# Performance work log

Hardware: AMD Instinct MI355X
Metric: run time of the kernel (lower is better)

## Reference

```python
import jax, jax.numpy as jnp
import numpy as np

K = 2            # negative:positive edge ratio (init arg k)
N_NODES = 4096
N_EDGES = 8192
FEAT = 64


def setup_inputs() -> dict:
    key = jax.random.key(0)
    k1, k2, k3 = jax.random.split(key, 3)
    node_feature = jax.random.normal(k1, (N_NODES, FEAT), dtype=jnp.float32)
    edge_src = jax.random.randint(k2, (N_EDGES,), 0, N_NODES, dtype=jnp.int32)
    edge_dst = jax.random.randint(k3, (N_EDGES,), 0, N_NODES, dtype=jnp.int32)
    return {"node_feature": node_feature, "edge_src": edge_src, "edge_dst": edge_dst}


def reference(node_feature, edge_src, edge_dst):
    E = edge_src.shape[0]
    N = node_feature.shape[0]
    # [E, E] pairwise mask: candidate column j is valid for row i iff
    # dst[j] != dst[i] and dst[j] != src[i]
    valid = (edge_dst[:, None] != edge_dst[None, :]) & (edge_src[:, None] != edge_dst[None, :])
    # unsorted_segment_min over rows grouped by edge_src -> [N, E]
    segmin = jax.ops.segment_min(valid.astype(jnp.int8), edge_src, num_segments=N)
    # gather back per edge -> [E, E], flatten
    m = segmin[edge_src].reshape(-1).astype(bool)  # [E*E]
    num_negatives = jnp.sum(m)
    ratio = num_negatives // E                      # integer ratio as in TF code
    keep_prob = (K / ratio).astype(jnp.float32)
    u = jax.random.uniform(jax.random.key(42), (E * E,), dtype=jnp.float32)
    keep = m & (u < keep_prob)
    # fixed-size (jit-friendly) stand-in for tf.boolean_mask: expected count is K*E;
    # pad/truncate to exactly K*E kept flat indices (fill_value=0 pads).
    idx = jnp.nonzero(keep, size=K * E, fill_value=0)[0]
    rows = idx // E
    cols = idx % E
    edge_src_neg = edge_src[rows]
    edge_dst_neg = edge_dst[cols]
    return edge_src_neg, edge_dst_neg
```

## Files before the change

### kernel.cpp

```cpp
#include <hip/hip_runtime.h>
#include <stdint.h>
#include <math.h>

typedef unsigned int u32;
typedef unsigned long long u64;

#define E_CNT   8192
#define N_CNT   4096
#define TOT_N   (1u << 26)
#define OUT_K   16384
#define NODE_BM_WORDS 128
#define N_CHUNKS 1024

#define OFF_BAD      0x000000
#define OFF_CNT_DST  0x200000
#define OFF_CNT_SRC  0x204000
#define OFF_CCOUNT   0x208000
#define OFF_SCALARS  0x209000
#define OFF_KEEPBM   0x210000
#define ZERO_BYTES   0x209040

__device__ __forceinline__ u32 rotl32(u32 x, u32 d) {
  return __builtin_amdgcn_alignbit(x, x, 32u - d);
}

__device__ __forceinline__ void threefry2_0_42(u32 ia, u32 ib, u32& bits_a, u32& bits_b) {
  const u32 k1 = 42u, k2 = 0x1BD11BF0u;
  u32 a0 = ia + k1, a1r;
  u32 b0 = ib + k1;
  u32 A0 = 0u, A1 = a0;
  u32 B0 = 0u, B1 = b0;
#define R2(r) { A0 += A1; B0 += B1; A1 = rotl32(A1, r); B1 = rotl32(B1, r); A1 ^= A0; B1 ^= B0; }
  R2(13) R2(15) R2(26) R2(6)
  A0 += k1; B0 += k1; A1 += k2 + 1u; B1 += k2 + 1u;
  R2(17) R2(29) R2(16) R2(24)
  A0 += k2; B0 += k2; A1 += 2u; B1 += 2u;
  R2(13) R2(15) R2(26) R2(6)
   A1 += k1 + 3u; B1 += k1 + 3u;
  R2(17) R2(29) R2(16) R2(24)
  A0 += k1; B0 += k1; A1 += k2 + 4u; B1 += k2 + 4u;
  R2(13) R2(15) R2(26) R2(6)
  A0 += k2; B0 += k2; A1 += 5u; B1 += 5u;
#undef R2
  bits_a = A0 ^ A1;
  bits_b = B0 ^ B1;
  (void)a1r;
}

__global__ void k_build(const int* __restrict__ src, const int* __restrict__ dst,
                        u32* __restrict__ bad, u32* __restrict__ cnt_dst,
                        u32* __restrict__ cnt_src, int* __restrict__ out) {
  int tid = blockIdx.x * 256 + threadIdx.x;
  if (tid < N_CNT) {
    atomicOr(&bad[(u32)tid * NODE_BM_WORDS + ((u32)tid >> 5)], 1u << (tid & 31));
  }
  u32 s = (u32)src[tid], d = (u32)dst[tid];
  atomicOr(&bad[s * NODE_BM_WORDS + (d >> 5)], 1u << (d & 31));
  atomicAdd(&cnt_dst[d], 1u);
  atomicAdd(&cnt_src[s], 1u);
  int s0 = src[0], d0 = dst[0];
  out[tid] = s0;            out[tid + E_CNT] = s0;
  out[OUT_K + tid] = d0;    out[OUT_K + tid + E_CNT] = d0;
}

__global__ void __launch_bounds__(1024) k_rowcount(const u32* __restrict__ bad,
                                                   const u32* __restrict__ cnt_dst,
                                                   const u32* __restrict__ cnt_src,
                                                   u32* __restrict__ scal) {
  int wv = threadIdx.x >> 6, ln = threadIdx.x & 63;
  int n = blockIdx.x * 16 + wv;
  const u32* row = bad + (u32)n * NODE_BM_WORDS;
  u32 sum = 0;
#pragma unroll
  for (int h = 0; h < 2; ++h) {
    int w = ln + h * 64;
    u32 bits = row[w];
    while (bits) { int b = __ffs(bits) - 1; sum += cnt_dst[(w << 5) + b]; bits &= bits - 1; }
  }
#pragma unroll
  for (int off = 32; off > 0; off >>= 1) sum += __shfl_down(sum, off, 64);
  __shared__ u32 part[16];
  if (ln == 0) part[wv] = ((u32)E_CNT - sum) * cnt_src[n];
  __syncthreads();
  if (threadIdx.x == 0) {
    u32 tot = 0;
#pragma unroll
    for (int k = 0; k < 16; ++k) tot += part[k];
    atomicAdd(&scal[0], tot);
    __threadfence();
    if (atomicAdd(&scal[1], 1u) == 255u) {
      u32 nn = atomicAdd(&scal[0], 0u);
      u32 ratio = nn >> 13;
      float kp = 2.0f / (float)ratio;
      u32 T = (u32)ceil((double)kp * 8388608.0);
      u32 T9 = (T >= (1u << 23)) ? 0xFFFFFFFFu : (T << 9);
      atomicExch(&scal[2], T9);
    }
  }
}

__global__ void __launch_bounds__(256) k_sample(const int* __restrict__ src,
                                                const int* __restrict__ dst,
                                                const u32* __restrict__ bad,
                                                const u32* __restrict__ scal,
                                                u64* __restrict__ keep_bm,
                                                u32* __restrict__ ccount) {
  u32 wv = threadIdx.x >> 6, ln = threadIdx.x & 63;
  u32 i0w = blockIdx.x * 2048u + wv * 512u;
  u32 T9 = scal[2];
  u64 words[8];
  u64 any = 0;
#pragma unroll
  for (int j = 0; j < 4; ++j) {
    u32 ia = i0w + (u32)j * 128u + ln;
    u32 ba, bb;
    threefry2_0_42(ia, ia + 64u, ba, bb);
    u64 ma = __ballot(ba < T9);
    u64 mb = __ballot(bb < T9);
    words[2 * j] = ma; words[2 * j + 1] = mb;
    any |= ma | mb;
  }
  if (any) {
#pragma unroll
    for (int k = 0; k < 8; ++k) {
      if (words[k]) {
        u32 i = i0w + (u32)k * 64u + ln;
        bool kp = (words[k] >> ln) & 1ull;
        if (kp) {
          u32 n = (u32)src[i >> 13]; u32 v = (u32)dst[i & 8191];
          kp = ((bad[n * NODE_BM_WORDS + (v >> 5)] >> (v & 31)) & 1u) == 0u;
        }
        words[k] = __ballot(kp);
      }
    }
  }
  if (ln == 0) {
    u32 widx = i0w >> 6;
    ulonglong2* p = (ulonglong2*)&keep_bm[widx];
    p[0] = make_ulonglong2(words[0], words[1]);
    p[1] = make_ulonglong2(words[2], words[3]);
    p[2] = make_ulonglong2(words[4], words[5]);
    p[3] = make_ulonglong2(words[6], words[7]);
    u32 c = 0;
#pragma unroll
    for (int k = 0; k < 8; ++k) c += (u32)__popcll(words[k]);
    if (c) atomicAdd(&ccount[i0w >> 16], c);
  }
}

__global__ void k_compact(const int* __restrict__ src, const int* __restrict__ dst,
                          const u64* __restrict__ keep_bm, const u32* __restrict__ ccount,
                          int* __restrict__ out) {
  int c = blockIdx.x;
  int t = threadIdx.x;
  __shared__ u32 s[256];
  __shared__ u32 base_sh;

  u32 v[4]; u32 sum4 = 0;
#pragma unroll
  for (int k = 0; k < 4; ++k) { v[k] = ccount[4 * t + k]; sum4 += v[k]; }
  s[t] = sum4; __syncthreads();
  for (int off = 1; off < 256; off <<= 1) {
    u32 x = (t >= off) ? s[t - off] : 0u;
    __syncthreads();
    s[t] += x;
    __syncthreads();
  }
  if (t == (c >> 2)) {
    u32 excl = s[t] - sum4;
#pragma unroll
    for (int k = 0; k < 4; ++k) if (k < (c & 3)) excl += v[k];
    base_sh = excl;
  }
  __syncthreads();
  u32 coff_c = base_sh;
  __syncthreads();

  const u64* words = keep_bm + (size_t)c * 1024;
  u64 w[4];
  u32 cnt = 0;
#pragma unroll
  for (int k = 0; k < 4; ++k) { w[k] = words[4 * t + k]; cnt += (u32)__popcll(w[k]); }
  s[t] = cnt; __syncthreads();
  for (int off = 1; off < 256; off <<= 1) {
    u32 x = (t >= off) ? s[t - off] : 0u;
    __syncthreads();
    s[t] += x;
    __syncthreads();
  }
  u32 rank = coff_c + s[t] - cnt;
  u32 tbase = (u32)c * 65536u + (u32)t * 256u;
#pragma unroll
  for (int k = 0; k < 4; ++k) {
    u64 bits = w[k];
    while (bits) {
      int b = __ffsll((unsigned long long)bits) - 1;
      if (rank < OUT_K) {
        u32 tt = tbase + (u32)k * 64u + (u32)b;
        out[rank]         = src[tt >> 13];
        out[OUT_K + rank] = dst[tt & 8191];
      }
      rank++;
      bits &= bits - 1;
    }
  }
}

extern "C" void kernel_launch(void* const* d_in, const int* in_sizes, int n_in,
                              void* d_out, int out_size, void* d_ws, size_t ws_size,
                              hipStream_t stream) {
  const int* src = (const int*)d_in[1];
  const int* dst = (const int*)d_in[2];
  int* out = (int*)d_out;
  char* ws = (char*)d_ws;

  u32* bad     = (u32*)(ws + OFF_BAD);
  u32* cnt_dst = (u32*)(ws + OFF_CNT_DST);
  u32* cnt_src = (u32*)(ws + OFF_CNT_SRC);
  u32* ccount  = (u32*)(ws + OFF_CCOUNT);
  u32* scal    = (u32*)(ws + OFF_SCALARS);
  u64* keep_bm = (u64*)(ws + OFF_KEEPBM);

  hipMemsetAsync(ws, 0, ZERO_BYTES, stream);
  k_build<<<E_CNT / 256, 256, 0, stream>>>(src, dst, bad, cnt_dst, cnt_src, out);
  k_rowcount<<<N_CNT / 16, 1024, 0, stream>>>(bad, cnt_dst, cnt_src, scal);
  k_sample<<<TOT_N / 2048, 256, 0, stream>>>(src, dst, bad, scal, keep_bm, ccount);
  k_compact<<<N_CHUNKS, 256, 0, stream>>>(src, dst, keep_bm, ccount, out);
}
```

Baseline: 189.1 us.

## Fuse build, rowcount, sample and compact into one persistent kernel with grid barriers

```diff
diff --git a/kernel.cpp b/kernel.cpp
--- a/kernel.cpp
+++ b/kernel.cpp
@@ -7,10 +7,11 @@
 
 #define E_CNT   8192
 #define N_CNT   4096
-#define TOT_N   (1u << 26)
 #define OUT_K   16384
 #define NODE_BM_WORDS 128
-#define N_CHUNKS 1024
+#define NB      512
+#define NT      1024
+#define ELEMS_PER_BLOCK 131072u
 
 #define OFF_BAD      0x000000
 #define OFF_CNT_DST  0x200000
@@ -18,7 +19,7 @@
 #define OFF_CCOUNT   0x208000
 #define OFF_SCALARS  0x209000
 #define OFF_KEEPBM   0x210000
-#define ZERO_BYTES   0x209040
+#define ZERO_WORDS   (0x208000 / 4)
 
 __device__ __forceinline__ u32 rotl32(u32 x, u32 d) {
   return __builtin_amdgcn_alignbit(x, x, 32u - d);
@@ -26,17 +27,15 @@
 
 __device__ __forceinline__ void threefry2_0_42(u32 ia, u32 ib, u32& bits_a, u32& bits_b) {
   const u32 k1 = 42u, k2 = 0x1BD11BF0u;
-  u32 a0 = ia + k1, a1r;
-  u32 b0 = ib + k1;
-  u32 A0 = 0u, A1 = a0;
-  u32 B0 = 0u, B1 = b0;
+  u32 A0 = 0u, A1 = ia + k1;
+  u32 B0 = 0u, B1 = ib + k1;
 #define R2(r) { A0 += A1; B0 += B1; A1 = rotl32(A1, r); B1 = rotl32(B1, r); A1 ^= A0; B1 ^= B0; }
   R2(13) R2(15) R2(26) R2(6)
   A0 += k1; B0 += k1; A1 += k2 + 1u; B1 += k2 + 1u;
   R2(17) R2(29) R2(16) R2(24)
   A0 += k2; B0 += k2; A1 += 2u; B1 += 2u;
   R2(13) R2(15) R2(26) R2(6)
-   A1 += k1 + 3u; B1 += k1 + 3u;
+  A1 += k1 + 3u; B1 += k1 + 3u;
   R2(17) R2(29) R2(16) R2(24)
   A0 += k1; B0 += k1; A1 += k2 + 4u; B1 += k2 + 4u;
   R2(13) R2(15) R2(26) R2(6)
@@ -44,51 +43,95 @@
 #undef R2
   bits_a = A0 ^ A1;
   bits_b = B0 ^ B1;
-  (void)a1r;
-}
-
-__global__ void k_build(const int* __restrict__ src, const int* __restrict__ dst,
-                        u32* __restrict__ bad, u32* __restrict__ cnt_dst,
-                        u32* __restrict__ cnt_src, int* __restrict__ out) {
-  int tid = blockIdx.x * 256 + threadIdx.x;
-  if (tid < N_CNT) {
-    atomicOr(&bad[(u32)tid * NODE_BM_WORDS + ((u32)tid >> 5)], 1u << (tid & 31));
-  }
-  u32 s = (u32)src[tid], d = (u32)dst[tid];
-  atomicOr(&bad[s * NODE_BM_WORDS + (d >> 5)], 1u << (d & 31));
-  atomicAdd(&cnt_dst[d], 1u);
-  atomicAdd(&cnt_src[s], 1u);
-  int s0 = src[0], d0 = dst[0];
-  out[tid] = s0;            out[tid + E_CNT] = s0;
-  out[OUT_K + tid] = d0;    out[OUT_K + tid + E_CNT] = d0;
-}
-
-__global__ void __launch_bounds__(1024) k_rowcount(const u32* __restrict__ bad,
-                                                   const u32* __restrict__ cnt_dst,
-                                                   const u32* __restrict__ cnt_src,
-                                                   u32* __restrict__ scal) {
-  int wv = threadIdx.x >> 6, ln = threadIdx.x & 63;
-  int n = blockIdx.x * 16 + wv;
-  const u32* row = bad + (u32)n * NODE_BM_WORDS;
-  u32 sum = 0;
-#pragma unroll
-  for (int h = 0; h < 2; ++h) {
-    int w = ln + h * 64;
-    u32 bits = row[w];
-    while (bits) { int b = __ffs(bits) - 1; sum += cnt_dst[(w << 5) + b]; bits &= bits - 1; }
-  }
-#pragma unroll
-  for (int off = 32; off > 0; off >>= 1) sum += __shfl_down(sum, off, 64);
+}
+
+__device__ __forceinline__ void gbar(u32* bar) {
+  __syncthreads();
+  if (threadIdx.x == 0) {
+    __threadfence();
+    atomicAdd(bar, 1u);
+    while (atomicAdd(bar, 0u) < (u32)NB) __builtin_amdgcn_s_sleep(2);
+    __threadfence();
+  }
+  __syncthreads();
+}
+
+__device__ __forceinline__ u32 block_scan(u32 v, u32* s) {
+  int t = threadIdx.x;
+  s[t] = v; __syncthreads();
+  for (int off = 1; off < NT; off <<= 1) {
+    u32 x = (t >= off) ? s[t - off] : 0u;
+    __syncthreads();
+    s[t] += x;
+    __syncthreads();
+  }
+  u32 r = s[t];
+  __syncthreads();
+  return r;
+}
+
+__global__ void __launch_bounds__(NT, 8) k_all(const int* __restrict__ src,
+                                               const int* __restrict__ dst,
+                                               u32* __restrict__ ws32,
+                                               u64* __restrict__ keep_bm,
+                                               int* __restrict__ out) {
+  u32* bad     = ws32 + (OFF_BAD >> 2);
+  u32* cnt_dst = ws32 + (OFF_CNT_DST >> 2);
+  u32* cnt_src = ws32 + (OFF_CNT_SRC >> 2);
+  u32* ccount  = ws32 + (OFF_CCOUNT >> 2);
+  u32* scal    = ws32 + (OFF_SCALARS >> 2);
+  u32* bars    = scal + 3;
+
+  const u32 b = blockIdx.x, t = threadIdx.x;
+  const u32 wv = t >> 6, ln = t & 63;
+  const u32 g = b * NT + t;
+
+  __shared__ u32 s[NT];
   __shared__ u32 part[16];
-  if (ln == 0) part[wv] = ((u32)E_CNT - sum) * cnt_src[n];
-  __syncthreads();
-  if (threadIdx.x == 0) {
+  __shared__ u32 wsum[16];
+  __shared__ u32 sh_t9;
+  __shared__ u32 chunk_off[2];
+
+  ws32[g] = 0;
+  if (g < (u32)(ZERO_WORDS - NB * NT)) ws32[NB * NT + g] = 0;
+  gbar(&bars[0]);
+
+  if (g < N_CNT) atomicOr(&bad[g * NODE_BM_WORDS + (g >> 5)], 1u << (g & 31));
+  if (g < E_CNT) {
+    u32 sv = (u32)src[g], dv = (u32)dst[g];
+    atomicOr(&bad[sv * NODE_BM_WORDS + (dv >> 5)], 1u << (dv & 31));
+    atomicAdd(&cnt_dst[dv], 1u);
+    atomicAdd(&cnt_src[sv], 1u);
+    int s0 = src[0], d0 = dst[0];
+    out[g] = s0;           out[g + E_CNT] = s0;
+    out[OUT_K + g] = d0;   out[OUT_K + g + E_CNT] = d0;
+  }
+  gbar(&bars[1]);
+
+  if (t < 16) part[t] = 0;
+  __syncthreads();
+  u32 gw = b * 16 + wv;
+  if (gw < N_CNT) {
+    const u32* row = bad + gw * NODE_BM_WORDS;
+    u32 sum = 0;
+#pragma unroll
+    for (int h = 0; h < 2; ++h) {
+      u32 w = ln + h * 64u;
+      u32 bits = row[w];
+      while (bits) { int bb = __ffs(bits) - 1; sum += cnt_dst[(w << 5) + bb]; bits &= bits - 1; }
+    }
+#pragma unroll
+    for (int off = 32; off > 0; off >>= 1) sum += __shfl_down(sum, off, 64);
+    if (ln == 0) part[wv] = ((u32)E_CNT - sum) * cnt_src[gw];
+  }
+  __syncthreads();
+  if (t == 0) {
     u32 tot = 0;
 #pragma unroll
     for (int k = 0; k < 16; ++k) tot += part[k];
-    atomicAdd(&scal[0], tot);
+    if (tot) atomicAdd(&scal[0], tot);
     __threadfence();
-    if (atomicAdd(&scal[1], 1u) == 255u) {
+    if (atomicAdd(&scal[1], 1u) == (u32)(NB - 1)) {
       u32 nn = atomicAdd(&scal[0], 0u);
       u32 ratio = nn >> 13;
       float kp = 2.0f / (float)ratio;
@@ -97,111 +140,85 @@
       atomicExch(&scal[2], T9);
     }
   }
-}
-
-__global__ void __launch_bounds__(256) k_sample(const int* __restrict__ src,
-                                                const int* __restrict__ dst,
-                                                const u32* __restrict__ bad,
-                                                const u32* __restrict__ scal,
-                                                u64* __restrict__ keep_bm,
-                                                u32* __restrict__ ccount) {
-  u32 wv = threadIdx.x >> 6, ln = threadIdx.x & 63;
-  u32 i0w = blockIdx.x * 2048u + wv * 512u;
-  u32 T9 = scal[2];
-  u64 words[8];
-  u64 any = 0;
-#pragma unroll
-  for (int j = 0; j < 4; ++j) {
-    u32 ia = i0w + (u32)j * 128u + ln;
-    u32 ba, bb;
-    threefry2_0_42(ia, ia + 64u, ba, bb);
-    u64 ma = __ballot(ba < T9);
-    u64 mb = __ballot(bb < T9);
-    words[2 * j] = ma; words[2 * j + 1] = mb;
-    any |= ma | mb;
-  }
-  if (any) {
-#pragma unroll
-    for (int k = 0; k < 8; ++k) {
-      if (words[k]) {
-        u32 i = i0w + (u32)k * 64u + ln;
-        bool kp = (words[k] >> ln) & 1ull;
-        if (kp) {
-          u32 n = (u32)src[i >> 13]; u32 v = (u32)dst[i & 8191];
-          kp = ((bad[n * NODE_BM_WORDS + (v >> 5)] >> (v & 31)) & 1u) == 0u;
+  gbar(&bars[2]);
+  if (t == 0) sh_t9 = atomicAdd(&scal[2], 0u);
+  __syncthreads();
+  const u32 T9 = sh_t9;
+
+  const u32 eb = b * ELEMS_PER_BLOCK + wv * 8192u;
+  u32 wave_c = 0;
+  for (int it = 0; it < 16; ++it) {
+    u32 i0w = eb + (u32)it * 512u;
+    u64 words[8];
+    u64 any = 0;
+#pragma unroll
+    for (int j = 0; j < 4; ++j) {
+      u32 ia = i0w + (u32)j * 128u + ln;
+      u32 ba, bb;
+      threefry2_0_42(ia, ia + 64u, ba, bb);
+      u64 ma = __ballot(ba < T9);
+      u64 mb = __ballot(bb < T9);
+      words[2 * j] = ma; words[2 * j + 1] = mb;
+      any |= ma | mb;
+    }
+    if (any) {
+#pragma unroll
+      for (int k = 0; k < 8; ++k) {
+        if (words[k]) {
+          u32 i = i0w + (u32)k * 64u + ln;
+          bool kp = (words[k] >> ln) & 1ull;
+          if (kp) {
+            u32 n = (u32)src[i >> 13]; u32 v = (u32)dst[i & 8191];
+            kp = ((bad[n * NODE_BM_WORDS + (v >> 5)] >> (v & 31)) & 1u) == 0u;
+          }
+          words[k] = __ballot(kp);
         }
-        words[k] = __ballot(kp);
       }
     }
-  }
-  if (ln == 0) {
-    u32 widx = i0w >> 6;
-    ulonglong2* p = (ulonglong2*)&keep_bm[widx];
-    p[0] = make_ulonglong2(words[0], words[1]);
-    p[1] = make_ulonglong2(words[2], words[3]);
-    p[2] = make_ulonglong2(words[4], words[5]);
-    p[3] = make_ulonglong2(words[6], words[7]);
-    u32 c = 0;
-#pragma unroll
-    for (int k = 0; k < 8; ++k) c += (u32)__popcll(words[k]);
-    if (c) atomicAdd(&ccount[i0w >> 16], c);
-  }
-}
-
-__global__ void k_compact(const int* __restrict__ src, const int* __restrict__ dst,
-                          const u64* __restrict__ keep_bm, const u32* __restrict__ ccount,
-                          int* __restrict__ out) {
-  int c = blockIdx.x;
-  int t = threadIdx.x;
-  __shared__ u32 s[256];
-  __shared__ u32 base_sh;
-
-  u32 v[4]; u32 sum4 = 0;
-#pragma unroll
-  for (int k = 0; k < 4; ++k) { v[k] = ccount[4 * t + k]; sum4 += v[k]; }
-  s[t] = sum4; __syncthreads();
-  for (int off = 1; off < 256; off <<= 1) {
-    u32 x = (t >= off) ? s[t - off] : 0u;
-    __syncthreads();
-    s[t] += x;
-    __syncthreads();
-  }
-  if (t == (c >> 2)) {
-    u32 excl = s[t] - sum4;
-#pragma unroll
-    for (int k = 0; k < 4; ++k) if (k < (c & 3)) excl += v[k];
-    base_sh = excl;
-  }
-  __syncthreads();
-  u32 coff_c = base_sh;
-  __syncthreads();
-
-  const u64* words = keep_bm + (size_t)c * 1024;
-  u64 w[4];
-  u32 cnt = 0;
-#pragma unroll
-  for (int k = 0; k < 4; ++k) { w[k] = words[4 * t + k]; cnt += (u32)__popcll(w[k]); }
-  s[t] = cnt; __syncthreads();
-  for (int off = 1; off < 256; off <<= 1) {
-    u32 x = (t >= off) ? s[t - off] : 0u;
-    __syncthreads();
-    s[t] += x;
-    __syncthreads();
-  }
-  u32 rank = coff_c + s[t] - cnt;
-  u32 tbase = (u32)c * 65536u + (u32)t * 256u;
-#pragma unroll
-  for (int k = 0; k < 4; ++k) {
-    u64 bits = w[k];
-    while (bits) {
-      int b = __ffsll((unsigned long long)bits) - 1;
+    if (ln == 0) {
+      ulonglong2* p = (ulonglong2*)&keep_bm[i0w >> 6];
+      p[0] = make_ulonglong2(words[0], words[1]);
+      p[1] = make_ulonglong2(words[2], words[3]);
+      p[2] = make_ulonglong2(words[4], words[5]);
+      p[3] = make_ulonglong2(words[6], words[7]);
+      u32 c = 0;
+#pragma unroll
+      for (int k = 0; k < 8; ++k) c += (u32)__popcll(words[k]);
+      wave_c += c;
+    }
+  }
+  if (ln == 0) wsum[wv] = wave_c;
+  __syncthreads();
+  if (t < 2) {
+    u32 cs = 0;
+#pragma unroll
+    for (int k = 0; k < 8; ++k) cs += wsum[t * 8 + k];
+    ccount[b * 2 + t] = cs;
+  }
+  gbar(&bars[3]);
+
+  u32 cval = ccount[t];
+  u32 incl = block_scan(cval, s);
+  if (t == 2 * b)     chunk_off[0] = incl - cval;
+  if (t == 2 * b + 1) chunk_off[1] = incl - cval;
+  __syncthreads();
+#pragma unroll
+  for (int k = 0; k < 2; ++k) {
+    u32 c = 2 * b + (u32)k;
+    u64 w = keep_bm[c * 1024u + t];
+    u32 pc = (u32)__popcll(w);
+    u32 incl2 = block_scan(pc, s);
+    u32 rank = chunk_off[k] + incl2 - pc;
+    u32 tt0 = (c << 16) + (t << 6);
+    while (w) {
+      int bb = __ffsll((unsigned long long)w) - 1;
       if (rank < OUT_K) {
-        u32 tt = tbase + (u32)k * 64u + (u32)b;
+        u32 tt = tt0 + (u32)bb;
         out[rank]         = src[tt >> 13];
         out[OUT_K + rank] = dst[tt & 8191];
       }
       rank++;
-      bits &= bits - 1;
+      w &= w - 1;
     }
   }
 }
@@ -214,16 +231,6 @@
   int* out = (int*)d_out;
   char* ws = (char*)d_ws;
 
-  u32* bad     = (u32*)(ws + OFF_BAD);
-  u32* cnt_dst = (u32*)(ws + OFF_CNT_DST);
-  u32* cnt_src = (u32*)(ws + OFF_CNT_SRC);
-  u32* ccount  = (u32*)(ws + OFF_CCOUNT);
-  u32* scal    = (u32*)(ws + OFF_SCALARS);
-  u64* keep_bm = (u64*)(ws + OFF_KEEPBM);
-
-  hipMemsetAsync(ws, 0, ZERO_BYTES, stream);
-  k_build<<<E_CNT / 256, 256, 0, stream>>>(src, dst, bad, cnt_dst, cnt_src, out);
-  k_rowcount<<<N_CNT / 16, 1024, 0, stream>>>(bad, cnt_dst, cnt_src, scal);
-  k_sample<<<TOT_N / 2048, 256, 0, stream>>>(src, dst, bad, scal, keep_bm, ccount);
-  k_compact<<<N_CHUNKS, 256, 0, stream>>>(src, dst, keep_bm, ccount, out);
-}
+  hipMemsetAsync(ws + OFF_SCALARS, 0, 64, stream);
+  k_all<<<NB, NT, 0, stream>>>(src, dst, (u32*)ws, (u64*)(ws + OFF_KEEPBM), out);
+}
```

Result: slower. 407.4 us (+115.4%).
